# Kernel optimization log

Measured on AMD Instinct MI355X. Metric: run time of the kernel, lower is better.

Reference implementation:

```python
import jax, jax.numpy as jnp
import numpy as np

N = 50000
E = 400000
F_IN = 128
NUM_CLASSES = 16
# (heads, out_channels, concat) per GATConv layer
LAYERS = [(8, 32, True), (8, 16, True), (8, 8, True), (1, NUM_CLASSES, False)]
DIMS_IN = [F_IN, 256, 128, 64]
NEG_SLOPE = 0.2
BN_EPS = 1e-5


def setup_inputs() -> dict:
    key = jax.random.key(0)
    ks = iter(jax.random.split(key, 64))
    inp = {}
    inp["x"] = jax.random.normal(next(ks), (N, F_IN), dtype=jnp.float32)
    inp["src"] = jax.random.randint(next(ks), (E,), 0, N, dtype=jnp.int32)
    inp["dst"] = jax.random.randint(next(ks), (E,), 0, N, dtype=jnp.int32)
    for l, ((h, c, concat), din) in enumerate(zip(LAYERS, DIMS_IN), start=1):
        s = 1.0 / np.sqrt(din)
        inp[f"W{l}"] = jax.random.normal(next(ks), (din, h * c), dtype=jnp.float32) * s
        inp[f"asrc{l}"] = jax.random.normal(next(ks), (h, c), dtype=jnp.float32) * 0.1
        inp[f"adst{l}"] = jax.random.normal(next(ks), (h, c), dtype=jnp.float32) * 0.1
        dout = h * c if concat else c
        inp[f"b{l}"] = jax.random.normal(next(ks), (dout,), dtype=jnp.float32) * 0.01
        inp[f"g{l}"] = jax.random.uniform(next(ks), (dout,), dtype=jnp.float32, minval=0.5, maxval=1.5)
        inp[f"be{l}"] = jax.random.normal(next(ks), (dout,), dtype=jnp.float32) * 0.1
        inp[f"rm{l}"] = jax.random.normal(next(ks), (dout,), dtype=jnp.float32) * 0.1
        inp[f"rv{l}"] = jax.random.uniform(next(ks), (dout,), dtype=jnp.float32, minval=0.5, maxval=1.5)
    return inp


def _gat_conv(x, src, dst, W, a_src, a_dst, bias, heads, ch, concat):
    n = x.shape[0]
    h = (x @ W).reshape(n, heads, ch)                     # [N,H,C]
    e_s = jnp.einsum('nhc,hc->nh', h, a_src)              # [N,H]
    e_d = jnp.einsum('nhc,hc->nh', h, a_dst)
    alpha = jax.nn.leaky_relu(e_s[src] + e_d[dst], NEG_SLOPE)   # [E,H]
    amax = jax.ops.segment_max(alpha, dst, num_segments=n)
    ex = jnp.exp(alpha - amax[dst])
    den = jax.ops.segment_sum(ex, dst, num_segments=n)
    attn = ex / (den[dst] + 1e-16)                        # [E,H]
    out = jax.ops.segment_sum(h[src] * attn[:, :, None], dst, num_segments=n)  # [N,H,C]
    out = out.reshape(n, heads * ch) if concat else out.mean(axis=1)
    return out + bias


def _bn(x, g, b, rm, rv):
    return (x - rm) * jax.lax.rsqrt(rv + BN_EPS) * g + b


def _forward(x, src, dst, params):
    # PyG GATConv adds self-loops by default
    loops = jnp.arange(N, dtype=src.dtype)
    s = jnp.concatenate([src, loops])
    d = jnp.concatenate([dst, loops])
    out = x
    for l, (h, c, concat) in enumerate(LAYERS, start=1):
        W, a_s, a_d, b, g, be, rm, rv = (params[f"{k}{l}"] for k in
                                         ("W", "asrc", "adst", "b", "g", "be", "rm", "rv"))
        out = _gat_conv(out, s, d, W, a_s, a_d, b, h, c, concat)
        if l < 4:
            out = jax.nn.elu(out)
        out = _bn(out, g, be, rm, rv)
    return out


def reference(x, src, dst,
              W1, asrc1, adst1, b1, g1, be1, rm1, rv1,
              W2, asrc2, adst2, b2, g2, be2, rm2, rv2,
              W3, asrc3, adst3, b3, g3, be3, rm3, rv3,
              W4, asrc4, adst4, b4, g4, be4, rm4, rv4):
    params = dict(
        W1=W1, asrc1=asrc1, adst1=adst1, b1=b1, g1=g1, be1=be1, rm1=rm1, rv1=rv1,
        W2=W2, asrc2=asrc2, adst2=adst2, b2=b2, g2=g2, be2=be2, rm2=rm2, rv2=rv2,
        W3=W3, asrc3=asrc3, adst3=adst3, b3=b3, g3=g3, be3=be3, rm3=rm3, rv3=rv3,
        W4=W4, asrc4=asrc4, adst4=adst4, b4=b4, g4=g4, be4=be4, rm4=rm4, rv4=rv4)
    return _forward(x, src, dst, params)
```

## Files before the change

### kernel.cpp

```cpp
#include <hip/hip_runtime.h>

#define NEG_SLOPE 0.2f
#define BN_EPS 1e-5f

typedef unsigned short u16;
typedef unsigned int u32;
typedef __bf16 bf16x8 __attribute__((ext_vector_type(8)));
typedef float f32x4 __attribute__((ext_vector_type(4)));

__device__ __forceinline__ u32 f2bf(float f) {
    u32 u = __float_as_uint(f);
    return (u + 0x7FFFu + ((u >> 16) & 1u)) >> 16;
}
__device__ __forceinline__ float bf2f(u32 h) { return __uint_as_float(h << 16); }
__device__ __forceinline__ float bfl(u32 p) { return __uint_as_float(p << 16); }
__device__ __forceinline__ float bfh(u32 p) { return __uint_as_float(p & 0xFFFF0000u); }

__device__ __forceinline__ void split8(const float4 f0, const float4 f1, uint4& vh, uint4& vl) {
    float f[8] = {f0.x, f0.y, f0.z, f0.w, f1.x, f1.y, f1.z, f1.w};
    u32 h[8], l[8];
    #pragma unroll
    for (int i = 0; i < 8; i++) { h[i] = f2bf(f[i]); l[i] = f2bf(f[i] - bf2f(h[i])); }
    vh = make_uint4(h[0] | (h[1] << 16), h[2] | (h[3] << 16), h[4] | (h[5] << 16), h[6] | (h[7] << 16));
    vl = make_uint4(l[0] | (l[1] << 16), l[2] | (l[3] << 16), l[4] | (l[5] << 16), l[6] | (l[7] << 16));
}

__global__ void wt_prep3(const float* __restrict__ W1, const float* __restrict__ W2,
                         const float* __restrict__ W3,
                         u16* __restrict__ h1, u16* __restrict__ l1,
                         u16* __restrict__ h2, u16* __restrict__ l2,
                         u16* __restrict__ h3, u16* __restrict__ l3) {
    int i = blockIdx.x * blockDim.x + threadIdx.x;
    const float* W; u16 *ph, *pl; int K, N, off;
    if (i < 32768)      { W = W1; ph = h1; pl = l1; K = 128; N = 256; off = i; }
    else if (i < 65536) { W = W2; ph = h2; pl = l2; K = 256; N = 128; off = i - 32768; }
    else if (i < 73728) { W = W3; ph = h3; pl = l3; K = 128; N = 64;  off = i - 65536; }
    else return;
    int k = off / N, n = off - k * N;
    float w = W[off];
    u32 h = f2bf(w);
    ph[n * K + k] = (u16)h;
    pl[n * K + k] = (u16)f2bf(w - bf2f(h));
}

template<int BN, int HMC, int AF32>
__launch_bounds__(256)
__global__ void gemm_mfma(const void* __restrict__ A_, const u16* __restrict__ Alo,
                          const u16* __restrict__ Bhi, const u16* __restrict__ Blo,
                          u16* __restrict__ Cbf, int M, int K, int N) {
    constexpr int FM = (BN == 128) ? 4 : 2;
    __shared__ uint4 sA[2][512];
    __shared__ uint4 sB[2][BN * 4];
    const int tid = threadIdx.x;
    const int bm = blockIdx.y * 128;
    const int bn = blockIdx.x * BN;
    const int lane = tid & 63;
    const int w = tid >> 6;
    const int wm = (BN == 128) ? (w >> 1) * 64 : w * 32;
    const int wn = (BN == 128) ? (w & 1) * 64 : 0;
    const int fr = lane & 15;
    const int fs = lane >> 4;
    f32x4 zero = {0.f, 0.f, 0.f, 0.f};
    f32x4 acc[FM][4];
    #pragma unroll
    for (int i = 0; i < FM; i++)
        #pragma unroll
        for (int j = 0; j < 4; j++) acc[i][j] = zero;

    const int r0 = tid >> 2;
    const int ss = tid & 3;
    const int r1 = r0 + 64;
    const int d0 = r0 * 4 + (ss ^ ((r0 >> 1) & 3));
    const int d1 = r1 * 4 + (ss ^ ((r1 >> 1) & 3));

    for (int k0 = 0; k0 < K; k0 += 32) {
        if constexpr (AF32) {
            const float* Af = (const float*)A_;
            int gr = bm + r0;
            uint4 vh = make_uint4(0,0,0,0), vl = make_uint4(0,0,0,0);
            if (gr < M) {
                float4 f0 = *(const float4*)(Af + (size_t)gr * K + k0 + ss * 8);
                float4 f1 = *(const float4*)(Af + (size_t)gr * K + k0 + ss * 8 + 4);
                split8(f0, f1, vh, vl);
            }
            sA[0][d0] = vh; sA[1][d0] = vl;
            gr = bm + r1;
            vh = make_uint4(0,0,0,0); vl = make_uint4(0,0,0,0);
            if (gr < M) {
                float4 f0 = *(const float4*)(Af + (size_t)gr * K + k0 + ss * 8);
                float4 f1 = *(const float4*)(Af + (size_t)gr * K + k0 + ss * 8 + 4);
                split8(f0, f1, vh, vl);
            }
            sA[0][d1] = vh; sA[1][d1] = vl;
        } else {
            const u16* Ahi = (const u16*)A_;
            int gr = bm + r0;
            uint4 vh = make_uint4(0,0,0,0), vl = make_uint4(0,0,0,0);
            if (gr < M) {
                vh = *(const uint4*)(Ahi + (size_t)gr * K + k0 + ss * 8);
                vl = *(const uint4*)(Alo + (size_t)gr * K + k0 + ss * 8);
            }
            sA[0][d0] = vh; sA[1][d0] = vl;
            gr = bm + r1;
            vh = make_uint4(0,0,0,0); vl = make_uint4(0,0,0,0);
            if (gr < M) {
                vh = *(const uint4*)(Ahi + (size_t)gr * K + k0 + ss * 8);
                vl = *(const uint4*)(Alo + (size_t)gr * K + k0 + ss * 8);
            }
            sA[0][d1] = vh; sA[1][d1] = vl;
        }
        {
            int gr = bn + r0;
            sB[0][d0] = *(const uint4*)(Bhi + (size_t)gr * K + k0 + ss * 8);
            sB[1][d0] = *(const uint4*)(Blo + (size_t)gr * K + k0 + ss * 8);
            if constexpr (BN == 128) {
                gr = bn + r1;
                sB[0][d1] = *(const uint4*)(Bhi + (size_t)gr * K + k0 + ss * 8);
                sB[1][d1] = *(const uint4*)(Blo + (size_t)gr * K + k0 + ss * 8);
            }
        }
        __syncthreads();
        bf16x8 ah[FM], al[FM], bh[4], bl[4];
        #pragma unroll
        for (int mi = 0; mi < FM; mi++) {
            int row = wm + mi * 16 + fr;
            int idx = row * 4 + (fs ^ ((row >> 1) & 3));
            ah[mi] = *reinterpret_cast<const bf16x8*>(&sA[0][idx]);
            al[mi] = *reinterpret_cast<const bf16x8*>(&sA[1][idx]);
        }
        #pragma unroll
        for (int ni = 0; ni < 4; ni++) {
            int row = wn + ni * 16 + fr;
            int idx = row * 4 + (fs ^ ((row >> 1) & 3));
            bh[ni] = *reinterpret_cast<const bf16x8*>(&sB[0][idx]);
            bl[ni] = *reinterpret_cast<const bf16x8*>(&sB[1][idx]);
        }
        #pragma unroll
        for (int mi = 0; mi < FM; mi++)
            #pragma unroll
            for (int ni = 0; ni < 4; ni++) {
                acc[mi][ni] = __builtin_amdgcn_mfma_f32_16x16x32_bf16(ah[mi], bh[ni], acc[mi][ni], 0, 0, 0);
                acc[mi][ni] = __builtin_amdgcn_mfma_f32_16x16x32_bf16(ah[mi], bl[ni], acc[mi][ni], 0, 0, 0);
                acc[mi][ni] = __builtin_amdgcn_mfma_f32_16x16x32_bf16(al[mi], bh[ni], acc[mi][ni], 0, 0, 0);
            }
        __syncthreads();
    }
    #pragma unroll
    for (int mi = 0; mi < FM; mi++) {
        #pragma unroll
        for (int ni = 0; ni < 4; ni++) {
            int colg = bn + wn + ni * 16 + fr;
            int rbase = bm + wm + mi * 16 + fs * 4;
            #pragma unroll
            for (int r = 0; r < 4; r++) {
                int rw = rbase + r;
                if (rw >= M) continue;
                u16 val = (u16)f2bf(acc[mi][ni][r]);
                if constexpr (HMC > 0) {
                    int hh2 = colg / HMC, cc2 = colg - hh2 * HMC;
                    Cbf[((size_t)hh2 * M + rw) * HMC + cc2] = val;
                } else {
                    Cbf[(size_t)rw * N + colg] = val;
                }
            }
        }
    }
}

__launch_bounds__(256)
__global__ void gemm_k64n16(const float* __restrict__ A, const float* __restrict__ B,
                            u16* __restrict__ Cbf, int M) {
    __shared__ float As[64][68];
    __shared__ float Bs[64][16];
    const int tid = threadIdx.x;
    const int bm = blockIdx.x * 64;
    {
        int r = tid >> 2, c = (tid & 3) << 2;
        *reinterpret_cast<float4*>(&Bs[r][c]) = *reinterpret_cast<const float4*>(&B[r * 16 + c]);
    }
    #pragma unroll
    for (int p = 0; p < 4; p++) {
        int m = (tid >> 4) + p * 16;
        int c = (tid & 15) << 2;
        int gm = bm + m;
        float4 v = make_float4(0.f, 0.f, 0.f, 0.f);
        if (gm < M) v = *reinterpret_cast<const float4*>(&A[(size_t)gm * 64 + c]);
        *reinterpret_cast<float4*>(&As[m][c]) = v;
    }
    __syncthreads();
    const int tc = tid & 15;
    const int r0 = tid >> 4;
    float acc[4] = {};
    #pragma unroll
    for (int k4 = 0; k4 < 16; k4++) {
        float b0 = Bs[4 * k4 + 0][tc];
        float b1 = Bs[4 * k4 + 1][tc];
        float b2 = Bs[4 * k4 + 2][tc];
        float b3 = Bs[4 * k4 + 3][tc];
        #pragma unroll
        for (int i = 0; i < 4; i++) {
            float4 av = *reinterpret_cast<const float4*>(&As[r0 + i * 16][4 * k4]);
            acc[i] += av.x * b0 + av.y * b1 + av.z * b2 + av.w * b3;
        }
    }
    #pragma unroll
    for (int i = 0; i < 4; i++) {
        int m = bm + r0 + i * 16;
        if (m < M) Cbf[(size_t)m * 16 + tc] = (u16)f2bf(acc[i]);
    }
}

__global__ void scores_kernel(const u16* __restrict__ h,
                              const float* __restrict__ asrc,
                              const float* __restrict__ adst,
                              float* __restrict__ es, float* __restrict__ ed,
                              int Nn, int H, int C) {
    int idx = blockIdx.x * blockDim.x + threadIdx.x;
    if (idx >= Nn * H) return;
    int n = idx / H, hh = idx % H;
    const u16* hp = h + ((size_t)hh * Nn + n) * C;
    const float4* ap = reinterpret_cast<const float4*>(asrc + hh * C);
    const float4* bp = reinterpret_cast<const float4*>(adst + hh * C);
    float s = 0.f, d = 0.f;
    for (int c4 = 0; c4 < C / 4; c4++) {
        uint2 pv = *reinterpret_cast<const uint2*>(hp + 4 * c4);
        float v0 = bfl(pv.x), v1 = bfh(pv.x), v2 = bfl(pv.y), v3 = bfh(pv.y);
        float4 a = ap[c4], b = bp[c4];
        s += v0 * a.x + v1 * a.y + v2 * a.z + v3 * a.w;
        d += v0 * b.x + v1 * b.y + v2 * b.z + v3 * b.w;
    }
    es[(size_t)hh * Nn + n] = s;
    ed[(size_t)hh * Nn + n] = d;
}

__global__ void hist_kernel(const int* __restrict__ dst, int* __restrict__ counts,
                            int E0, int Etot) {
    int e = blockIdx.x * blockDim.x + threadIdx.x;
    if (e >= Etot) return;
    int d_ = (e < E0) ? dst[e] : e - E0;
    atomicAdd(&counts[d_], 1);
}

__global__ void scan_kernel(int* __restrict__ counts, int* __restrict__ row_ptr, int Nn) {
    __shared__ int wsum[16];
    __shared__ int chunk_total;
    __shared__ int carry_s;
    const int tid = threadIdx.x;
    const int lane = tid & 63;
    const int wid = tid >> 6;
    if (tid == 0) carry_s = 0;
    __syncthreads();
    for (int base = 0; base < Nn; base += 1024) {
        int i = base + tid;
        int v = (i < Nn) ? counts[i] : 0;
        int iv = v;
        #pragma unroll
        for (int off = 1; off < 64; off <<= 1) {
            int t = __shfl_up(iv, off, 64);
            if (lane >= off) iv += t;
        }
        if (lane == 63) wsum[wid] = iv;
        __syncthreads();
        if (tid == 0) {
            int s = 0;
            #pragma unroll
            for (int k = 0; k < 16; k++) { int t = wsum[k]; wsum[k] = s; s += t; }
            chunk_total = s;
        }
        __syncthreads();
        if (i < Nn) {
            int ex = carry_s + wsum[wid] + (iv - v);
            row_ptr[i] = ex;
            counts[i] = ex;
        }
        __syncthreads();
        if (tid == 0) carry_s += chunk_total;
        __syncthreads();
    }
    if (tid == 0) row_ptr[Nn] = carry_s;
}

__global__ void scatter_kernel(const int* __restrict__ src, const int* __restrict__ dst,
                               int* __restrict__ cursor, int* __restrict__ col,
                               int E0, int Etot) {
    int e = blockIdx.x * blockDim.x + threadIdx.x;
    if (e >= Etot) return;
    int d_ = (e < E0) ? dst[e] : e - E0;
    int s_ = (e < E0) ? src[e] : e - E0;
    int pos = atomicAdd(&cursor[d_], 1);
    col[pos] = s_;
}

template<int H, int C, int NT, int DO_ELU, int OUT_HILO>
__launch_bounds__(256)
__global__ void gat_fused(const int* __restrict__ row_ptr, const int* __restrict__ col,
                          const float* __restrict__ es, const float* __restrict__ ed,
                          const u16* __restrict__ h16, float* __restrict__ outf,
                          u16* __restrict__ outh, u16* __restrict__ outl,
                          const float* __restrict__ bias, const float* __restrict__ g,
                          const float* __restrict__ be, const float* __restrict__ rm,
                          const float* __restrict__ rv, int Nn) {
    constexpr int Dout = H * C;
    constexpr int VEC = C / NT;
    constexpr int NPB = 256 / NT;
    const int tid = threadIdx.x;
    const int bx = blockIdx.x;
    const int hh = (H == 8) ? (bx & 7) : 0;
    const int nb = (H == 8) ? (bx >> 3) : bx;
    const int node = nb * NPB + tid / NT;
    const int t = tid % NT;
    if (node >= Nn) return;
    const int jb = row_ptr[node], je = row_ptr[node + 1];
    const float* esh = es + (size_t)hh * Nn;
    const float edv = ed[(size_t)hh * Nn + node];
    const u16* hb = h16 + (size_t)hh * Nn * C + t * VEC;
    float acc[VEC] = {};
    float den = 0.f;
    int j = jb;
    for (; j + 4 <= je; j += 4) {
        int s0 = col[j], s1 = col[j + 1], s2 = col[j + 2], s3 = col[j + 3];
        float e0 = esh[s0] + edv, e1 = esh[s1] + edv, e2 = esh[s2] + edv, e3 = esh[s3] + edv;
        e0 = (e0 >= 0.f) ? e0 : NEG_SLOPE * e0;
        e1 = (e1 >= 0.f) ? e1 : NEG_SLOPE * e1;
        e2 = (e2 >= 0.f) ? e2 : NEG_SLOPE * e2;
        e3 = (e3 >= 0.f) ? e3 : NEG_SLOPE * e3;
        float w0 = __expf(e0), w1 = __expf(e1), w2 = __expf(e2), w3 = __expf(e3);
        den += (w0 + w1) + (w2 + w3);
        if constexpr (VEC == 8) {
            uint4 p0 = *reinterpret_cast<const uint4*>(hb + (size_t)s0 * C);
            uint4 p1 = *reinterpret_cast<const uint4*>(hb + (size_t)s1 * C);
            uint4 p2 = *reinterpret_cast<const uint4*>(hb + (size_t)s2 * C);
            uint4 p3 = *reinterpret_cast<const uint4*>(hb + (size_t)s3 * C);
            acc[0] += w0 * bfl(p0.x) + w1 * bfl(p1.x) + w2 * bfl(p2.x) + w3 * bfl(p3.x);
            acc[1] += w0 * bfh(p0.x) + w1 * bfh(p1.x) + w2 * bfh(p2.x) + w3 * bfh(p3.x);
            acc[2] += w0 * bfl(p0.y) + w1 * bfl(p1.y) + w2 * bfl(p2.y) + w3 * bfl(p3.y);
            acc[3] += w0 * bfh(p0.y) + w1 * bfh(p1.y) + w2 * bfh(p2.y) + w3 * bfh(p3.y);
            acc[4] += w0 * bfl(p0.z) + w1 * bfl(p1.z) + w2 * bfl(p2.z) + w3 * bfl(p3.z);
            acc[5] += w0 * bfh(p0.z) + w1 * bfh(p1.z) + w2 * bfh(p2.z) + w3 * bfh(p3.z);
            acc[6] += w0 * bfl(p0.w) + w1 * bfl(p1.w) + w2 * bfl(p2.w) + w3 * bfl(p3.w);
            acc[7] += w0 * bfh(p0.w) + w1 * bfh(p1.w) + w2 * bfh(p2.w) + w3 * bfh(p3.w);
        } else {
            uint2 p0 = *reinterpret_cast<const uint2*>(hb + (size_t)s0 * C);
            uint2 p1 = *reinterpret_cast<const uint2*>(hb + (size_t)s1 * C);
            uint2 p2 = *reinterpret_cast<const uint2*>(hb + (size_t)s2 * C);
            uint2 p3 = *reinterpret_cast<const uint2*>(hb + (size_t)s3 * C);
            acc[0] += w0 * bfl(p0.x) + w1 * bfl(p1.x) + w2 * bfl(p2.x) + w3 * bfl(p3.x);
            acc[1] += w0 * bfh(p0.x) + w1 * bfh(p1.x) + w2 * bfh(p2.x) + w3 * bfh(p3.x);
            acc[2] += w0 * bfl(p0.y) + w1 * bfl(p1.y) + w2 * bfl(p2.y) + w3 * bfl(p3.y);
            acc[3] += w0 * bfh(p0.y) + w1 * bfh(p1.y) + w2 * bfh(p2.y) + w3 * bfh(p3.y);
        }
    }
    for (; j < je; j++) {
        int s = col[j];
        float a = esh[s] + edv;
        a = (a >= 0.f) ? a : NEG_SLOPE * a;
        float w = __expf(a);
        den += w;
        if constexpr (VEC == 8) {
            uint4 pv = *reinterpret_cast<const uint4*>(hb + (size_t)s * C);
            acc[0] += w * bfl(pv.x); acc[1] += w * bfh(pv.x);
            acc[2] += w * bfl(pv.y); acc[3] += w * bfh(pv.y);
            acc[4] += w * bfl(pv.z); acc[5] += w * bfh(pv.z);
            acc[6] += w * bfl(pv.w); acc[7] += w * bfh(pv.w);
        } else {
            uint2 pv = *reinterpret_cast<const uint2*>(hb + (size_t)s * C);
            acc[0] += w * bfl(pv.x); acc[1] += w * bfh(pv.x);
            acc[2] += w * bfl(pv.y); acc[3] += w * bfh(pv.y);
        }
    }
    const float inv = 1.f / (den + 1e-16f);
    const int jc = hh * C + t * VEC;
    float res[VEC];
    #pragma unroll
    for (int v = 0; v < VEC; v++) {
        float y = acc[v] * inv + bias[jc + v];
        if (DO_ELU) y = (y > 0.f) ? y : expm1f(y);
        y = (y - rm[jc + v]) * rsqrtf(rv[jc + v] + BN_EPS) * g[jc + v] + be[jc + v];
        res[v] = y;
    }
    if constexpr (OUT_HILO) {
        u32 rh[VEC], rl[VEC];
        #pragma unroll
        for (int v = 0; v < VEC; v++) {
            rh[v] = f2bf(res[v]);
            rl[v] = f2bf(res[v] - bf2f(rh[v]));
        }
        if constexpr (VEC == 8) {
            uint4 ph = make_uint4(rh[0] | (rh[1] << 16), rh[2] | (rh[3] << 16),
                                  rh[4] | (rh[5] << 16), rh[6] | (rh[7] << 16));
            uint4 pl = make_uint4(rl[0] | (rl[1] << 16), rl[2] | (rl[3] << 16),
                                  rl[4] | (rl[5] << 16), rl[6] | (rl[7] << 16));
            *reinterpret_cast<uint4*>(outh + (size_t)node * Dout + jc) = ph;
            *reinterpret_cast<uint4*>(outl + (size_t)node * Dout + jc) = pl;
        } else {
            uint2 ph = make_uint2(rh[0] | (rh[1] << 16), rh[2] | (rh[3] << 16));
            uint2 pl = make_uint2(rl[0] | (rl[1] << 16), rl[2] | (rl[3] << 16));
            *reinterpret_cast<uint2*>(outh + (size_t)node * Dout + jc) = ph;
            *reinterpret_cast<uint2*>(outl + (size_t)node * Dout + jc) = pl;
        }
    } else {
        float* op = outf + (size_t)node * Dout + jc;
        if constexpr (VEC == 8) {
            *reinterpret_cast<float4*>(op) = make_float4(res[0], res[1], res[2], res[3]);
            *reinterpret_cast<float4*>(op + 4) = make_float4(res[4], res[5], res[6], res[7]);
        } else {
            *reinterpret_cast<float4*>(op) = make_float4(res[0], res[1], res[2], res[3]);
        }
    }
}

extern "C" void kernel_launch(void* const* d_in, const int* in_sizes, int n_in,
                              void* d_out, int out_size, void* d_ws, size_t ws_size,
                              hipStream_t stream) {
    const float* x = (const float*)d_in[0];
    const int* src = (const int*)d_in[1];
    const int* dst = (const int*)d_in[2];
    const int Nn = in_sizes[0] / 128;
    const int E0 = in_sizes[1];
    const int Etot = E0 + Nn;

    u16* A0 = (u16*)d_ws;
    u16* Bh = A0 + (size_t)Nn * 512;
    u16* Ch = Bh + (size_t)Nn * 256;
    float* es = (float*)(Ch + (size_t)Nn * 256);
    float* ed = es + (size_t)Nn * 8;
    int* row_ptr = (int*)(ed + (size_t)Nn * 8);
    int* cursor  = row_ptr + (Nn + 1);
    int* col     = cursor + Nn;
    u16* wth1 = (u16*)(col + Etot);
    u16* wtl1 = wth1 + 32768;
    u16* wth2 = wtl1 + 32768;
    u16* wtl2 = wth2 + 32768;
    u16* wth3 = wtl2 + 32768;
    u16* wtl3 = wth3 + 8192;

    u16* Y1H = A0;
    u16* Y1L = A0 + (size_t)Nn * 256;
    u16* Y2H = Ch;
    u16* Y2L = Ch + (size_t)Nn * 128;
    float* out3 = (float*)A0;

    hipMemsetAsync(cursor, 0, sizeof(int) * Nn, stream);
    hist_kernel<<<(Etot + 255) / 256, 256, 0, stream>>>(dst, cursor, E0, Etot);
    scan_kernel<<<1, 1024, 0, stream>>>(cursor, row_ptr, Nn);
    scatter_kernel<<<(Etot + 255) / 256, 256, 0, stream>>>(src, dst, cursor, col, E0, Etot);

    const int gy128 = (Nn + 127) / 128;

    const float* const* p1 = (const float* const*)(d_in + 3);
    const float* const* p2 = (const float* const*)(d_in + 11);
    const float* const* p3 = (const float* const*)(d_in + 19);
    const float* const* p4 = (const float* const*)(d_in + 27);

    wt_prep3<<<288, 256, 0, stream>>>(p1[0], p2[0], p3[0], wth1, wtl1, wth2, wtl2, wth3, wtl3);

    gemm_mfma<128, 32, 1><<<dim3(2, gy128), 256, 0, stream>>>(x, nullptr, wth1, wtl1, Bh, Nn, 128, 256);
    scores_kernel<<<(Nn * 8 + 255) / 256, 256, 0, stream>>>(Bh, p1[1], p1[2], es, ed, Nn, 8, 32);
    gat_fused<8, 32, 4, 1, 1><<<dim3(((Nn + 63) / 64) * 8), 256, 0, stream>>>(
        row_ptr, col, es, ed, Bh, nullptr, Y1H, Y1L, p1[3], p1[4], p1[5], p1[6], p1[7], Nn);

    gemm_mfma<128, 16, 0><<<dim3(1, gy128), 256, 0, stream>>>(Y1H, Y1L, wth2, wtl2, Bh, Nn, 256, 128);
    scores_kernel<<<(Nn * 8 + 255) / 256, 256, 0, stream>>>(Bh, p2[1], p2[2], es, ed, Nn, 8, 16);
    gat_fused<8, 16, 2, 1, 1><<<dim3(((Nn + 127) / 128) * 8), 256, 0, stream>>>(
        row_ptr, col, es, ed, Bh, nullptr, Y2H, Y2L, p2[3], p2[4], p2[5], p2[6], p2[7], Nn);

    gemm_mfma<64, 8, 0><<<dim3(1, gy128), 256, 0, stream>>>(Y2H, Y2L, wth3, wtl3, Bh, Nn, 128, 64);
    scores_kernel<<<(Nn * 8 + 255) / 256, 256, 0, stream>>>(Bh, p3[1], p3[2], es, ed, Nn, 8, 8);
    gat_fused<8, 8, 2, 1, 0><<<dim3(((Nn + 127) / 128) * 8), 256, 0, stream>>>(
        row_ptr, col, es, ed, Bh, out3, nullptr, nullptr, p3[3], p3[4], p3[5], p3[6], p3[7], Nn);

    gemm_k64n16<<<(Nn + 63) / 64, 256, 0, stream>>>(out3, p4[0], Bh, Nn);
    scores_kernel<<<(Nn + 255) / 256, 256, 0, stream>>>(Bh, p4[1], p4[2], es, ed, Nn, 1, 16);
    gat_fused<1, 16, 2, 0, 0><<<dim3((Nn + 127) / 128), 256, 0, stream>>>(
        row_ptr, col, es, ed, Bh, (float*)d_out, nullptr, nullptr, p4[3], p4[4], p4[5], p4[6], p4[7], Nn);
}
```

Before: 375.7 us.

## Sort nodes by in-degree to balance per-wavefront work in GAT aggregation

Adds a counting sort of nodes by in-degree (histogram, scan, scatter) and makes each gat_fused thread look up its node through the resulting permutation. Nodes of similar degree then share a wavefront, which is meant to reduce idle lanes caused by divergent neighbour-loop lengths. The cost is three extra small kernels plus a memset, atomic contention on 64 buckets, and loss of locality in node order for the ed reads and output writes.

```diff
diff --git a/kernel.cpp b/kernel.cpp
--- a/kernel.cpp
+++ b/kernel.cpp
@@ -2,6 +2,7 @@
 
 #define NEG_SLOPE 0.2f
 #define BN_EPS 1e-5f
+#define NDEG 64
 
 typedef unsigned short u16;
 typedef unsigned int u32;
@@ -291,9 +292,33 @@
     col[pos] = s_;
 }
 
+__global__ void deg_hist(const int* __restrict__ row_ptr, int* __restrict__ dbk, int Nn) {
+    int n = blockIdx.x * blockDim.x + threadIdx.x;
+    if (n >= Nn) return;
+    int d = row_ptr[n + 1] - row_ptr[n];
+    if (d > NDEG - 1) d = NDEG - 1;
+    atomicAdd(&dbk[d], 1);
+}
+__global__ void deg_scan(int* __restrict__ dbk, int* __restrict__ dcur) {
+    if (threadIdx.x == 0 && blockIdx.x == 0) {
+        int s = 0;
+        for (int i = 0; i < NDEG; i++) { int t = dbk[i]; dcur[i] = s; s += t; }
+    }
+}
+__global__ void deg_scatter(const int* __restrict__ row_ptr, int* __restrict__ dcur,
+                            int* __restrict__ perm, int Nn) {
+    int n = blockIdx.x * blockDim.x + threadIdx.x;
+    if (n >= Nn) return;
+    int d = row_ptr[n + 1] - row_ptr[n];
+    if (d > NDEG - 1) d = NDEG - 1;
+    int pos = atomicAdd(&dcur[d], 1);
+    perm[pos] = n;
+}
+
 template<int H, int C, int NT, int DO_ELU, int OUT_HILO>
 __launch_bounds__(256)
-__global__ void gat_fused(const int* __restrict__ row_ptr, const int* __restrict__ col,
+__global__ void gat_fused(const int* __restrict__ perm,
+                          const int* __restrict__ row_ptr, const int* __restrict__ col,
                           const float* __restrict__ es, const float* __restrict__ ed,
                           const u16* __restrict__ h16, float* __restrict__ outf,
                           u16* __restrict__ outh, u16* __restrict__ outl,
@@ -307,9 +332,10 @@
     const int bx = blockIdx.x;
     const int hh = (H == 8) ? (bx & 7) : 0;
     const int nb = (H == 8) ? (bx >> 3) : bx;
-    const int node = nb * NPB + tid / NT;
+    const int gid = nb * NPB + tid / NT;
     const int t = tid % NT;
-    if (node >= Nn) return;
+    if (gid >= Nn) return;
+    const int node = perm[gid];
     const int jb = row_ptr[node], je = row_ptr[node + 1];
     const float* esh = es + (size_t)hh * Nn;
     const float edv = ed[(size_t)hh * Nn + node];
@@ -433,6 +459,9 @@
     u16* wtl2 = wth2 + 32768;
     u16* wth3 = wtl2 + 32768;
     u16* wtl3 = wth3 + 8192;
+    int* perm = (int*)(wtl3 + 8192);
+    int* dbk  = perm + Nn;
+    int* dcur = dbk + NDEG;
 
     u16* Y1H = A0;
     u16* Y1L = A0 + (size_t)Nn * 256;
@@ -445,6 +474,11 @@
     scan_kernel<<<1, 1024, 0, stream>>>(cursor, row_ptr, Nn);
     scatter_kernel<<<(Etot + 255) / 256, 256, 0, stream>>>(src, dst, cursor, col, E0, Etot);
 
+    hipMemsetAsync(dbk, 0, sizeof(int) * NDEG, stream);
+    deg_hist<<<(Nn + 255) / 256, 256, 0, stream>>>(row_ptr, dbk, Nn);
+    deg_scan<<<1, 64, 0, stream>>>(dbk, dcur);
+    deg_scatter<<<(Nn + 255) / 256, 256, 0, stream>>>(row_ptr, dcur, perm, Nn);
+
     const int gy128 = (Nn + 127) / 128;
 
     const float* const* p1 = (const float* const*)(d_in + 3);
@@ -457,20 +491,20 @@
     gemm_mfma<128, 32, 1><<<dim3(2, gy128), 256, 0, stream>>>(x, nullptr, wth1, wtl1, Bh, Nn, 128, 256);
     scores_kernel<<<(Nn * 8 + 255) / 256, 256, 0, stream>>>(Bh, p1[1], p1[2], es, ed, Nn, 8, 32);
     gat_fused<8, 32, 4, 1, 1><<<dim3(((Nn + 63) / 64) * 8), 256, 0, stream>>>(
-        row_ptr, col, es, ed, Bh, nullptr, Y1H, Y1L, p1[3], p1[4], p1[5], p1[6], p1[7], Nn);
+        perm, row_ptr, col, es, ed, Bh, nullptr, Y1H, Y1L, p1[3], p1[4], p1[5], p1[6], p1[7], Nn);
 
     gemm_mfma<128, 16, 0><<<dim3(1, gy128), 256, 0, stream>>>(Y1H, Y1L, wth2, wtl2, Bh, Nn, 256, 128);
     scores_kernel<<<(Nn * 8 + 255) / 256, 256, 0, stream>>>(Bh, p2[1], p2[2], es, ed, Nn, 8, 16);
     gat_fused<8, 16, 2, 1, 1><<<dim3(((Nn + 127) / 128) * 8), 256, 0, stream>>>(
-        row_ptr, col, es, ed, Bh, nullptr, Y2H, Y2L, p2[3], p2[4], p2[5], p2[6], p2[7], Nn);
+        perm, row_ptr, col, es, ed, Bh, nullptr, Y2H, Y2L, p2[3], p2[4], p2[5], p2[6], p2[7], Nn);
 
     gemm_mfma<64, 8, 0><<<dim3(1, gy128), 256, 0, stream>>>(Y2H, Y2L, wth3, wtl3, Bh, Nn, 128, 64);
     scores_kernel<<<(Nn * 8 + 255) / 256, 256, 0, stream>>>(Bh, p3[1], p3[2], es, ed, Nn, 8, 8);
     gat_fused<8, 8, 2, 1, 0><<<dim3(((Nn + 127) / 128) * 8), 256, 0, stream>>>(
-        row_ptr, col, es, ed, Bh, out3, nullptr, nullptr, p3[3], p3[4], p3[5], p3[6], p3[7], Nn);
+        perm, row_ptr, col, es, ed, Bh, out3, nullptr, nullptr, p3[3], p3[4], p3[5], p3[6], p3[7], Nn);
 
     gemm_k64n16<<<(Nn + 63) / 64, 256, 0, stream>>>(out3, p4[0], Bh, Nn);
     scores_kernel<<<(Nn + 255) / 256, 256, 0, stream>>>(Bh, p4[1], p4[2], es, ed, Nn, 1, 16);
     gat_fused<1, 16, 2, 0, 0><<<dim3((Nn + 127) / 128), 256, 0, stream>>>(
-        row_ptr, col, es, ed, Bh, (float*)d_out, nullptr, nullptr, p4[3], p4[4], p4[5], p4[6], p4[7], Nn);
-}
+        perm, row_ptr, col, es, ed, Bh, (float*)d_out, nullptr, nullptr, p4[3], p4[4], p4[5], p4[6], p4[7], Nn);
+}
```

Measured after the change: 766.8 us. +104.1%, slower.
